# Kernel optimization log

Hardware: AMD Instinct MI355X
Metric: run time of the kernel (lower is better)

## Reference

```python
import jax, jax.numpy as jnp
import numpy as np

H_DIM = 1024
N_HEADS = 16
MAX_T = 2048
NUM_INPUTS = 3   # period of (return, state, action) tokens
RET_ORDER = 2


def _build_mask(T):
    # causal lower-triangular mask with mgdt selective column masking
    mask = jnp.tril(jnp.ones((T, T), dtype=bool))
    # columns period+ret_order-1, period+ret_order-1+period, ... are zeroed
    cols = np.arange(NUM_INPUTS + RET_ORDER - 1, MAX_T, NUM_INPUTS)
    cols = cols[cols < T]
    mask = mask.at[:, cols].set(False)
    return mask  # [T, T] bool


def setup_inputs() -> dict:
    key = jax.random.key(0)
    ks = jax.random.split(key, 9)
    B, T, C = 2, 2048, H_DIM
    s = 1.0 / np.sqrt(C)
    return {
        "x": jax.random.normal(ks[0], (B, T, C), dtype=jnp.float32),
        "Wq": jax.random.normal(ks[1], (C, C), dtype=jnp.float32) * s,
        "bq": jnp.zeros((C,), dtype=jnp.float32),
        "Wk": jax.random.normal(ks[2], (C, C), dtype=jnp.float32) * s,
        "bk": jnp.zeros((C,), dtype=jnp.float32),
        "Wv": jax.random.normal(ks[3], (C, C), dtype=jnp.float32) * s,
        "bv": jnp.zeros((C,), dtype=jnp.float32),
        "Wp": jax.random.normal(ks[4], (C, C), dtype=jnp.float32) * s,
        "bp": jnp.zeros((C,), dtype=jnp.float32),
    }


def reference(x, Wq, bq, Wk, bk, Wv, bv, Wp, bp):
    B, T, C = x.shape
    N = N_HEADS
    D = C // N
    # QKV projections; weights stored (in, out) so x @ W
    q = (x @ Wq + bq).reshape(B, T, N, D).transpose(0, 2, 1, 3)  # [B,N,T,D]
    k = (x @ Wk + bk).reshape(B, T, N, D).transpose(0, 2, 1, 3)
    v = (x @ Wv + bv).reshape(B, T, N, D).transpose(0, 2, 1, 3)

    scale = 1.0 / np.sqrt(D).astype(np.float32)
    scores = jnp.einsum("bntd,bnsd->bnts", q, k) * scale  # [B,N,T,T]
    mask = _build_mask(T)  # [T,T]
    scores = jnp.where(mask[None, None], scores, -jnp.inf)
    attn = jax.nn.softmax(scores, axis=-1)
    out = jnp.einsum("bnts,bnsd->bntd", attn, v)  # [B,N,T,D]
    out = out.transpose(0, 2, 1, 3).reshape(B, T, C)
    return out @ Wp + bp
```

## Files before the change

### kernel.cpp

```cpp
#include <hip/hip_runtime.h>

#define AS_GLOBAL __attribute__((address_space(1)))
#define AS_LDS    __attribute__((address_space(3)))

typedef __bf16 bf16;
typedef __bf16 bf16x4 __attribute__((ext_vector_type(4)));
typedef __bf16 bf16x8 __attribute__((ext_vector_type(8)));
typedef float  f32x4  __attribute__((ext_vector_type(4)));
typedef unsigned short u16x8 __attribute__((ext_vector_type(8)));

__device__ __forceinline__ void gload16(const void* g, void* l) {
  __builtin_amdgcn_global_load_lds((const AS_GLOBAL unsigned int*)g,
                                   (AS_LDS unsigned int*)l, 16, 0, 0);
}

__device__ __forceinline__ void* swz(void* base, int row, int bytecol) {
  return (char*)base + row * 128 + (bytecol ^ ((row & 7) << 4));
}

__device__ __forceinline__ int keptcnt(int X) { return X - ((X - 2) < 0 ? 0 : (X - 2) / 3); }
__device__ __forceinline__ int ci2s(int ci) {
  return 3 * ((ci - 2) >> 1) + 2 + ((ci - 2) & 1);
}
__device__ __forceinline__ int ci2s_full(int ci) {
  return ci < 2 ? ci : ci2s(ci);
}

__global__ __launch_bounds__(256) void k_prep(const float* __restrict__ x,
                                              const float* __restrict__ Wq,
                                              const float* __restrict__ Wk,
                                              const float* __restrict__ Wv,
                                              const float* __restrict__ Wp,
                                              const float* __restrict__ bq,
                                              const float* __restrict__ bk,
                                              const float* __restrict__ bv,
                                              bf16* __restrict__ xb,
                                              bf16* __restrict__ wqkvT,
                                              bf16* __restrict__ wpT,
                                              float* __restrict__ bc) {
  int blk = blockIdx.x;
  if (blk < 2048) {
    int i = blk * 256 + threadIdx.x;
    const float4* p = (const float4*)(x + (size_t)i * 8);
    float4 a = p[0], b = p[1];
    bf16x8 v;
    v[0] = (bf16)a.x; v[1] = (bf16)a.y; v[2] = (bf16)a.z; v[3] = (bf16)a.w;
    v[4] = (bf16)b.x; v[5] = (bf16)b.y; v[6] = (bf16)b.z; v[7] = (bf16)b.w;
    *(bf16x8*)(xb + (size_t)i * 8) = v;
  } else if (blk < 4096) {
    int wblk = blk - 2048;
    int sel = wblk >> 9;
    const float* W = (sel == 0) ? Wq : (sel == 1) ? Wk : (sel == 2) ? Wv : Wp;
    bf16* dst = (sel < 3) ? (wqkvT + (size_t)sel * 1024 * 1024) : wpT;
    int lin = (wblk & 511) * 256 + threadIdx.x;
    int n = lin & 1023, kc = lin >> 10;
    bf16x8 v;
#pragma unroll
    for (int j = 0; j < 8; ++j) v[j] = (bf16)W[(size_t)(kc * 8 + j) * 1024 + n];
    *(bf16x8*)&dst[(size_t)n * 1024 + kc * 8] = v;
  } else {
    int i = (blk - 4096) * 256 + threadIdx.x;
    bc[i] = (i < 1024) ? bq[i] : (i < 2048 ? bk[i - 1024] : bv[i - 2048]);
  }
}

__global__ __launch_bounds__(256) void k_compact(const bf16* __restrict__ qkv,
                                                 bf16* __restrict__ vc) {
  __shared__ unsigned L[32 * 65];
  int blk = blockIdx.x;
  int tid = threadIdx.x;
  int bh = blk / 22, cc = blk % 22;
  int b = bh >> 4, h = bh & 15;
  int ci0 = cc * 64;
  int p = tid >> 3, d0 = (tid & 7) * 8;
  int s0 = ci2s_full(ci0 + 2 * p), s1 = ci2s_full(ci0 + 2 * p + 1);
  u16x8 e = {}, od = {};
  if (s0 < 2048)
    e = *(const u16x8*)&qkv[(size_t)(b * 2048 + s0) * 3072 + 2048 + h * 64 + d0];
  if (s1 < 2048)
    od = *(const u16x8*)&qkv[(size_t)(b * 2048 + s1) * 3072 + 2048 + h * 64 + d0];
#pragma unroll
  for (int k2 = 0; k2 < 8; ++k2)
    L[p * 65 + d0 + k2] = (unsigned)e[k2] | ((unsigned)od[k2] << 16);
  __syncthreads();
#pragma unroll
  for (int it = 0; it < 2; ++it) {
    int d = it * 32 + (tid >> 3), jg = tid & 7;
    unsigned q4[4];
#pragma unroll
    for (int jj = 0; jj < 4; ++jj) q4[jj] = L[(jg * 4 + jj) * 65 + d];
    *(uint4*)&vc[((size_t)bh * 64 + d) * 1408 + ci0 + jg * 8] = *(uint4*)q4;
  }
}

template <typename OutT, int TM, int TN, int BK>
__global__ __launch_bounds__(256) void k_gemm_bt(const bf16* __restrict__ A,
                                                 const bf16* __restrict__ Bt,
                                                 const float* __restrict__ bias,
                                                 OutT* __restrict__ C,
                                                 int K, int N) {
  constexpr int GR = BK / 8;
  constexpr int MF = TM / 32, NF = TN / 32, KF = BK / 32;
  __shared__ bf16 As[2][TM * BK];
  __shared__ bf16 Bs[2][TN * BK];
  const int tid = threadIdx.x;
  const int w = tid >> 6, l = tid & 63, g = l >> 4, c = l & 15;
  const int wr = w >> 1, wc = w & 1;
  int lin = blockIdx.y * gridDim.x + blockIdx.x;
  int chunk = (gridDim.x * gridDim.y) >> 3;
  int nl = (lin & 7) * chunk + (lin >> 3);
  const int row0 = (nl % gridDim.x) * TM, col0 = (nl / gridDim.x) * TN;
  f32x4 acc[MF][NF] = {};

  auto swzj = [&](int j, int r) {
    if constexpr (BK == 32) return j ^ ((r >> 1) & 3);
    else                    return j ^ (r & 7);
  };

  auto stage = [&](int buf, int k0) {
#pragma unroll
    for (int it = 0; it < (TM * GR) / 256; ++it) {
      int idx = it * 256 + tid;
      int r = idx / GR, j = idx % GR;
      gload16(A + (size_t)(row0 + r) * K + k0 + swzj(j, r) * 8, &As[buf][idx * 8]);
    }
#pragma unroll
    for (int it = 0; it < (TN * GR) / 256; ++it) {
      int idx = it * 256 + tid;
      int r = idx / GR, j = idx % GR;
      gload16(Bt + (size_t)(col0 + r) * K + k0 + swzj(j, r) * 8, &Bs[buf][idx * 8]);
    }
  };

  stage(0, 0);
  int cur = 0;
#pragma unroll 1
  for (int k0 = 0; k0 < K; k0 += BK) {
    __syncthreads();

    if (k0 + BK < K) stage(cur ^ 1, k0 + BK);

    bf16x8 af[MF][KF], bfr[NF][KF];
#pragma unroll
    for (int m = 0; m < MF; ++m) {
      int row = wr * (TM / 2) + m * 16 + c;
#pragma unroll
      for (int kk = 0; kk < KF; ++kk)
        af[m][kk] = *(const bf16x8*)&As[cur][row * BK + swzj(kk * 4 + g, row) * 8];
    }
#pragma unroll
    for (int n = 0; n < NF; ++n) {
      int row = wc * (TN / 2) + n * 16 + c;
#pragma unroll
      for (int kk = 0; kk < KF; ++kk)
        bfr[n][kk] = *(const bf16x8*)&Bs[cur][row * BK + swzj(kk * 4 + g, row) * 8];
    }
#pragma unroll
    for (int m = 0; m < MF; ++m)
#pragma unroll
      for (int n = 0; n < NF; ++n)
#pragma unroll
        for (int kk = 0; kk < KF; ++kk)
          acc[m][n] = __builtin_amdgcn_mfma_f32_16x16x32_bf16(af[m][kk], bfr[n][kk],
                                                              acc[m][n], 0, 0, 0);
    cur ^= 1;
  }

#pragma unroll
  for (int m = 0; m < MF; ++m) {
    int row = row0 + wr * (TM / 2) + m * 16 + g * 4;
#pragma unroll
    for (int n = 0; n < NF; ++n) {
      int col = col0 + wc * (TN / 2) + n * 16 + c;
      float bv = bias[col];
#pragma unroll
      for (int r = 0; r < 4; ++r) {
        float v = acc[m][n][r] + bv;
        C[(size_t)(row + r) * N + col] = (OutT)v;
      }
    }
  }
}

__global__ __launch_bounds__(256, 4) void k_attn(const bf16* __restrict__ qkv,
                                                 const bf16* __restrict__ vc,
                                                 bf16* __restrict__ att) {
  const int idx = blockIdx.x;
  const int slot = idx >> 8, j = idx & 255;
  const int r8 = j >> 5, bh = j & 31;
  const int b = bh >> 4, h = bh & 15;
  int qt;
  switch (slot) {
    case 0: qt = r8;       break;
    case 1: qt = 31 - r8;  break;
    case 2: qt = r8 + 8;   break;
    default: qt = 23 - r8; break;
  }

  const int tid = threadIdx.x;
  const int w = tid >> 6, l = tid & 63, g = l >> 4, c = l & 15;
  const int qw0 = qt * 64 + w * 16;
  const int qq = qw0 + c;

  const int nt = (keptcnt(qt * 64 + 64) + 63) >> 6;
  const int tmaskw = keptcnt(qw0 + 1) >> 6;

  __shared__ bf16 Ks[2][64 * 64];
  __shared__ bf16 Vs[2][64 * 64];
  __shared__ bf16 Plds[4][16 * 64];

  const bf16* vgc = vc + (size_t)bh * 64 * 1408;

  auto stage = [&](int buf, int t) {
    int s0 = t * 64;
#pragma unroll
    for (int it = 0; it < 2; ++it) {
      int ch = it * 256 + tid;
      int rr = ch >> 3, jj = (ch & 7) ^ (rr & 7);
      int s = ci2s_full(s0 + rr);
      s = (s < 2048) ? s : 0;
      gload16(qkv + (size_t)(b * 2048 + s) * 3072 + 1024 + h * 64 + jj * 8,
              &Ks[buf][ch * 8]);
      gload16(vgc + (size_t)rr * 1408 + s0 + jj * 8, &Vs[buf][ch * 8]);
    }
  };

  const float QSCL = 0.125f * 1.44269504f;
  const bf16* qb = qkv + (size_t)(b * 2048 + qq) * 3072 + h * 64 + g * 8;
  bf16x8 qf0 = *(const bf16x8*)qb;
  bf16x8 qf1 = *(const bf16x8*)(qb + 32);
#pragma unroll
  for (int jq = 0; jq < 8; ++jq) {
    qf0[jq] = (bf16)((float)qf0[jq] * QSCL);
    qf1[jq] = (bf16)((float)qf1[jq] * QSCL);
  }

  f32x4 o[4] = {};
  float mrow = -1e30f, ell = 0.f;

  stage(0, 0);

  int cur = 0;
#pragma unroll 1
  for (int t = 0; t < nt; ++t) {
    __syncthreads();

    if (t + 1 < nt) stage(cur ^ 1, t + 1);

    f32x4 ss[4] = {};
    __builtin_amdgcn_s_setprio(1);
#pragma unroll
    for (int st = 0; st < 4; ++st) {
      bf16x8 ka  = *(const bf16x8*)swz(&Ks[cur][0], st * 16 + c, g * 16);
      bf16x8 kb2 = *(const bf16x8*)swz(&Ks[cur][0], st * 16 + c, 64 + g * 16);
      ss[st] = __builtin_amdgcn_mfma_f32_16x16x32_bf16(ka,  qf0, ss[st], 0, 0, 0);
      ss[st] = __builtin_amdgcn_mfma_f32_16x16x32_bf16(kb2, qf1, ss[st], 0, 0, 0);
    }
    __builtin_amdgcn_s_setprio(0);

    float mloc = -1e30f;
    if (t >= tmaskw) {
#pragma unroll
      for (int st = 0; st < 4; ++st)
#pragma unroll
        for (int r = 0; r < 4; ++r) {
          int ci = t * 64 + st * 16 + g * 4 + r;
          int s = ci2s(ci);
          if (t == 0) s = (ci < 2) ? ci : s;
          float v = (s <= qq) ? ss[st][r] : -1e30f;
          ss[st][r] = v;
          mloc = fmaxf(mloc, v);
        }
    } else {
#pragma unroll
      for (int st = 0; st < 4; ++st)
#pragma unroll
        for (int r = 0; r < 4; ++r) mloc = fmaxf(mloc, ss[st][r]);
    }
    mloc = fmaxf(mloc, __shfl_xor(mloc, 16));
    mloc = fmaxf(mloc, __shfl_xor(mloc, 32));

    if (!__all(mloc - mrow <= 12.0f)) {
      float mn = fmaxf(mrow, mloc);
      float al = exp2f(mrow - mn);
      mrow = mn;
      ell *= al;
#pragma unroll
      for (int dc = 0; dc < 4; ++dc)
#pragma unroll
        for (int r = 0; r < 4; ++r) o[dc][r] *= al;
    }

    float rsum = 0.f;
#pragma unroll
    for (int st = 0; st < 4; ++st) {
      float p0 = exp2f(ss[st][0] - mrow);
      float p1 = exp2f(ss[st][1] - mrow);
      float p2 = exp2f(ss[st][2] - mrow);
      float p3 = exp2f(ss[st][3] - mrow);
      rsum += (p0 + p1) + (p2 + p3);
      bf16x4 pk = {(bf16)p0, (bf16)p1, (bf16)p2, (bf16)p3};
      *(bf16x4*)swz(&Plds[w][0], c, st * 32 + g * 8) = pk;
    }
    ell += rsum;

    asm volatile("s_waitcnt lgkmcnt(0)" ::: "memory");
    __builtin_amdgcn_sched_barrier(0);

    __builtin_amdgcn_s_setprio(1);
#pragma unroll
    for (int kk = 0; kk < 2; ++kk) {
      bf16x8 pf = *(const bf16x8*)swz(&Plds[w][0], c, kk * 64 + g * 16);
#pragma unroll
      for (int dc = 0; dc < 4; ++dc) {
        bf16x8 vf = *(const bf16x8*)swz(&Vs[cur][0], dc * 16 + c, kk * 64 + g * 16);
        o[dc] = __builtin_amdgcn_mfma_f32_16x16x32_bf16(vf, pf, o[dc], 0, 0, 0);
      }
    }
    __builtin_amdgcn_s_setprio(0);

    cur ^= 1;
  }

  float et = ell;
  et += __shfl_xor(et, 16);
  et += __shfl_xor(et, 32);
  float inv = 1.f / et;
#pragma unroll
  for (int dc = 0; dc < 4; ++dc) {
    bf16x4 ok4 = {(bf16)(o[dc][0] * inv), (bf16)(o[dc][1] * inv),
                  (bf16)(o[dc][2] * inv), (bf16)(o[dc][3] * inv)};
    *(bf16x4*)swz(&Plds[w][0], c, dc * 32 + g * 8) = ok4;
  }
  asm volatile("s_waitcnt lgkmcnt(0)" ::: "memory");
  __builtin_amdgcn_sched_barrier(0);
#pragma unroll
  for (int p = 0; p < 2; ++p) {
    int row = p * 8 + (l >> 3);
    bf16x8 vrow = *(const bf16x8*)swz(&Plds[w][0], row, (l & 7) * 16);
    *(bf16x8*)&att[(size_t)(b * 2048 + qt * 64 + w * 16 + row) * 1024 +
                   h * 64 + (l & 7) * 8] = vrow;
  }
}

extern "C" void kernel_launch(void* const* d_in, const int* in_sizes, int n_in,
                              void* d_out, int out_size, void* d_ws, size_t ws_size,
                              hipStream_t stream) {
  const float* x  = (const float*)d_in[0];
  const float* Wq = (const float*)d_in[1];
  const float* bq = (const float*)d_in[2];
  const float* Wk = (const float*)d_in[3];
  const float* bk = (const float*)d_in[4];
  const float* Wv = (const float*)d_in[5];
  const float* bv = (const float*)d_in[6];
  const float* Wp = (const float*)d_in[7];
  const float* bp = (const float*)d_in[8];
  float* out = (float*)d_out;

  char* ws = (char*)d_ws;
  const size_t MB = 1024 * 1024;
  bf16*  xb    = (bf16*)(ws);
  bf16*  wqkvT = (bf16*)(ws + 8 * MB);
  bf16*  wpT   = (bf16*)(ws + 14 * MB);
  float* bcat  = (float*)(ws + 16 * MB);
  bf16*  qkv   = (bf16*)(ws + 17 * MB);
  bf16*  vcb   = (bf16*)(ws + 41 * MB);
  bf16*  att   = xb;

  k_prep<<<4108, 256, 0, stream>>>(x, Wq, Wk, Wv, Wp, bq, bk, bv,
                                   xb, wqkvT, wpT, bcat);
  k_gemm_bt<bf16, 128, 128, 32><<<dim3(32, 24), 256, 0, stream>>>(
      xb, wqkvT, bcat, qkv, 1024, 3072);
  k_compact<<<704, 256, 0, stream>>>(qkv, vcb);
  k_attn<<<1024, 256, 0, stream>>>(qkv, vcb, att);
  k_gemm_bt<float, 64, 128, 64><<<dim3(64, 8), 256, 0, stream>>>(
      att, wpT, bp, out, 1024, 1024);
}
```

Before: 102.9 us.

## Split long causal attention query tiles across two blocks and merge partials

Query tiles 16-31 are now split along the KV dimension into two blocks that each process half the KV tiles. Each half writes unnormalized fp32 outputs plus running max and sum to workspace, and a new merge kernel combines them with the log-sum-exp rule. This replaces the old slot-based load-balancing order and aims to shorten the critical path of the longest tiles while raising block count. The cost is an extra kernel launch, fp32 partial traffic, and the loss of the previous interleaved scheduling of heavy and light tiles.

```diff
diff --git a/kernel.cpp b/kernel.cpp
--- a/kernel.cpp
+++ b/kernel.cpp
@@ -184,18 +184,16 @@
 
 __global__ __launch_bounds__(256, 4) void k_attn(const bf16* __restrict__ qkv,
                                                  const bf16* __restrict__ vc,
-                                                 bf16* __restrict__ att) {
+                                                 bf16* __restrict__ att,
+                                                 float* __restrict__ po,
+                                                 float* __restrict__ pml) {
   const int idx = blockIdx.x;
-  const int slot = idx >> 8, j = idx & 255;
-  const int r8 = j >> 5, bh = j & 31;
+  const int bh = idx & 31, j2 = idx >> 5;
   const int b = bh >> 4, h = bh & 15;
-  int qt;
-  switch (slot) {
-    case 0: qt = r8;       break;
-    case 1: qt = 31 - r8;  break;
-    case 2: qt = r8 + 8;   break;
-    default: qt = 23 - r8; break;
-  }
+  int qt, half = 0;
+  const bool split = (j2 >= 16);
+  if (!split) { qt = j2; }
+  else { int k = j2 - 16; qt = 16 + (k >> 1); half = k & 1; }
 
   const int tid = threadIdx.x;
   const int w = tid >> 6, l = tid & 63, g = l >> 4, c = l & 15;
@@ -204,6 +202,12 @@
 
   const int nt = (keptcnt(qt * 64 + 64) + 63) >> 6;
   const int tmaskw = keptcnt(qw0 + 1) >> 6;
+  int t0 = 0, t1 = nt, slot = 0;
+  if (split) {
+    int nth = nt >> 1;
+    if (half) t0 = nth; else t1 = nth;
+    slot = (bh * 16 + (qt - 16)) * 2 + half;
+  }
 
   __shared__ bf16 Ks[2][64 * 64];
   __shared__ bf16 Vs[2][64 * 64];
@@ -238,14 +242,14 @@
   f32x4 o[4] = {};
   float mrow = -1e30f, ell = 0.f;
 
-  stage(0, 0);
+  stage(0, t0);
 
   int cur = 0;
 #pragma unroll 1
-  for (int t = 0; t < nt; ++t) {
+  for (int t = t0; t < t1; ++t) {
     __syncthreads();
 
-    if (t + 1 < nt) stage(cur ^ 1, t + 1);
+    if (t + 1 < t1) stage(cur ^ 1, t + 1);
 
     f32x4 ss[4] = {};
     __builtin_amdgcn_s_setprio(1);
@@ -325,6 +329,20 @@
   float et = ell;
   et += __shfl_xor(et, 16);
   et += __shfl_xor(et, 32);
+
+  if (split) {
+    float* prow = po + ((size_t)slot * 64 + w * 16 + c) * 64;
+#pragma unroll
+    for (int dc = 0; dc < 4; ++dc)
+      *(f32x4*)(prow + dc * 16 + g * 4) = o[dc];
+    if (g == 0) {
+      float* pm = pml + ((size_t)slot * 64 + w * 16 + c) * 2;
+      pm[0] = mrow;
+      pm[1] = et;
+    }
+    return;
+  }
+
   float inv = 1.f / et;
 #pragma unroll
   for (int dc = 0; dc < 4; ++dc) {
@@ -340,6 +358,35 @@
     bf16x8 vrow = *(const bf16x8*)swz(&Plds[w][0], row, (l & 7) * 16);
     *(bf16x8*)&att[(size_t)(b * 2048 + qt * 64 + w * 16 + row) * 1024 +
                    h * 64 + (l & 7) * 8] = vrow;
+  }
+}
+
+__global__ __launch_bounds__(256) void k_merge(const float* __restrict__ po,
+                                               const float* __restrict__ pml,
+                                               bf16* __restrict__ att) {
+  int mb = blockIdx.x;
+  int bh = mb & 31, qi = mb >> 5;
+  int b = bh >> 4, h = bh & 15;
+  int t = threadIdx.x;
+  int row = t & 63, dg = t >> 6;
+  size_t slot0 = (size_t)(bh * 16 + qi) * 2;
+  size_t r0 = (slot0 * 64 + row) * 64, r1 = ((slot0 + 1) * 64 + row) * 64;
+  float m0 = pml[(slot0 * 64 + row) * 2],     l0 = pml[(slot0 * 64 + row) * 2 + 1];
+  float m1 = pml[((slot0 + 1) * 64 + row) * 2], l1 = pml[((slot0 + 1) * 64 + row) * 2 + 1];
+  float m = fmaxf(m0, m1);
+  float a0 = exp2f(m0 - m), a1 = exp2f(m1 - m);
+  float inv = 1.f / (a0 * l0 + a1 * l1);
+  int q = (16 + qi) * 64 + row;
+  bf16* dst = att + (size_t)(b * 2048 + q) * 1024 + h * 64 + dg * 16;
+#pragma unroll
+  for (int jd = 0; jd < 16; jd += 4) {
+    f32x4 v0 = *(const f32x4*)&po[r0 + dg * 16 + jd];
+    f32x4 v1 = *(const f32x4*)&po[r1 + dg * 16 + jd];
+    bf16x4 r;
+#pragma unroll
+    for (int i = 0; i < 4; ++i)
+      r[i] = (bf16)((a0 * v0[i] + a1 * v1[i]) * inv);
+    *(bf16x4*)(dst + jd) = r;
   }
 }
 
@@ -365,6 +412,8 @@
   float* bcat  = (float*)(ws + 16 * MB);
   bf16*  qkv   = (bf16*)(ws + 17 * MB);
   bf16*  vcb   = (bf16*)(ws + 41 * MB);
+  float* po    = (float*)(ws + 56 * MB);
+  float* pml   = (float*)(ws + 74 * MB);
   bf16*  att   = xb;
 
   k_prep<<<4108, 256, 0, stream>>>(x, Wq, Wk, Wv, Wp, bq, bk, bv,
@@ -372,7 +421,8 @@
   k_gemm_bt<bf16, 128, 128, 32><<<dim3(32, 24), 256, 0, stream>>>(
       xb, wqkvT, bcat, qkv, 1024, 3072);
   k_compact<<<704, 256, 0, stream>>>(qkv, vcb);
-  k_attn<<<1024, 256, 0, stream>>>(qkv, vcb, att);
+  k_attn<<<1536, 256, 0, stream>>>(qkv, vcb, att, po, pml);
+  k_merge<<<512, 256, 0, stream>>>(po, pml, att);
   k_gemm_bt<float, 64, 128, 64><<<dim3(64, 8), 256, 0, stream>>>(
       att, wpT, bp, out, 1024, 1024);
 }
```

Result: slower. 112.1 us (+8.9%).
